# Optimization experiments

Measured on AMD Instinct MI355X. Metric: run time of the kernel, lower is better.

Reference implementation:

```python
import jax, jax.numpy as jnp
import numpy as np

NULL = -1.0
HORIZON = 10   # tile(1, 10, 1) in the original
N_REGIONS = 16


def setup_inputs() -> dict:
    key = jax.random.key(0)
    k1, k2, k3 = jax.random.split(key, 3)
    B, T, N, F = 16, 288, 4096, 2
    x = jax.random.uniform(k1, (B, T, N, F), dtype=jnp.float32) * 100.0
    miss = jax.random.uniform(k2, (B, T, N, F)) < 0.05
    x = jnp.where(miss, NULL, x)
    cluster_id = jax.random.randint(k3, (N,), 0, N_REGIONS)
    return {"data_seq": x, "cluster_id": cluster_id}


def reference(data_seq, cluster_id):
    # data_seq: [B, T, N, F] -> take feature 0 -> [B, T, N]
    x = data_seq[..., 0]
    # invalid_to_nan + nan_to_global_avg == replace -1 entries by global mean of valid entries
    valid = x != NULL
    xz = jnp.where(valid, x, 0.0)
    gmean = jnp.sum(xz) / jnp.maximum(jnp.sum(valid.astype(x.dtype)), 1.0)
    x = jnp.where(valid, x, gmean)
    # mean over time, tiled over prediction horizon: [B, HORIZON, N]
    pred_speed = jnp.tile(jnp.mean(x, axis=1, keepdims=True), (1, HORIZON, 1))
    # per-region mean over nodes (fused segment-mean instead of python loop): [B, HORIZON, R]
    counts = jax.ops.segment_sum(jnp.ones((cluster_id.shape[0],), x.dtype),
                                 cluster_id, num_segments=N_REGIONS)      # [R]
    sums = jax.ops.segment_sum(pred_speed.transpose(2, 0, 1),             # [N, B, H]
                               cluster_id, num_segments=N_REGIONS)        # [R, B, H]
    regional = (sums / jnp.maximum(counts, 1.0)[:, None, None]).transpose(1, 2, 0)
    return pred_speed, regional
```

## Files before the change

kernel.cpp:

```cpp
#include <hip/hip_runtime.h>
#include <hip/hip_bf16.h>

#define BB 16
#define TT 288
#define NN 4096
#define FF 2
#define RR 16
#define HH 10
#define TC 8
#define TSTEP (TT / TC)
#define NBLK1 (8 * TC * BB)
#define NULLV (-1.0f)

__global__ __launch_bounds__(256) void k_partial(
    const float4* __restrict__ x4,
    float2* __restrict__ psum2, int2* __restrict__ pcnt2,
    float* __restrict__ bsum, unsigned int* __restrict__ bcnt) {
  const int tid = threadIdx.x;
  const int n0  = blockIdx.x * 512 + tid * 2;
  const int tc  = blockIdx.y;
  const int b   = blockIdx.z;

  const float4* p = x4 + ((size_t)(b * TT + tc * TSTEP) * NN + n0) / 2;
  float s0 = 0.0f, s1 = 0.0f;
  unsigned int c0 = 0, c1 = 0;
#pragma unroll 12
  for (int t = 0; t < TSTEP; ++t) {
    float4 v = p[(size_t)t * (NN / 2)];
    bool v0 = (v.x != NULLV);
    bool v1 = (v.z != NULLV);
    s0 += v0 ? v.x : 0.0f;  c0 += v0 ? 1u : 0u;
    s1 += v1 ? v.z : 0.0f;  c1 += v1 ? 1u : 0u;
  }
  const size_t o2 = (((size_t)tc * BB + b) * NN + n0) / 2;
  psum2[o2] = make_float2(s0, s1);
  pcnt2[o2] = make_int2((int)c0, (int)c1);

  float rs = s0 + s1;
  unsigned int rc = c0 + c1;
  for (int off = 32; off > 0; off >>= 1) {
    rs += __shfl_down(rs, off);
    rc += __shfl_down(rc, off);
  }
  __shared__ float sh_s[4];
  __shared__ unsigned int sh_c[4];
  const int wid = tid >> 6;
  if ((tid & 63) == 0) { sh_s[wid] = rs; sh_c[wid] = rc; }
  __syncthreads();
  if (tid == 0) {
    const int blk = (blockIdx.z * TC + blockIdx.y) * 8 + blockIdx.x;
    bsum[blk] = sh_s[0] + sh_s[1] + sh_s[2] + sh_s[3];
    bcnt[blk] = sh_c[0] + sh_c[1] + sh_c[2] + sh_c[3];
  }
}

__global__ __launch_bounds__(256) void k_pred(
    const float4* __restrict__ psum4, const int4* __restrict__ pcnt4,
    const float4* __restrict__ bsum4, const uint4* __restrict__ bcnt4,
    const int4* __restrict__ cluster4,
    float4* __restrict__ out4, float* __restrict__ rsB) {
  const int tid = threadIdx.x;
  const int blk = blockIdx.x;
  const int b   = blk >> 2;
  const int n0  = (blk & 3) * 1024 + tid * 4;

  float4 bs = bsum4[tid];
  uint4  bc = bcnt4[tid];
  float rs = bs.x + bs.y + bs.z + bs.w;
  unsigned int rc = bc.x + bc.y + bc.z + bc.w;
  for (int off = 32; off > 0; off >>= 1) {
    rs += __shfl_down(rs, off);
    rc += __shfl_down(rc, off);
  }
  __shared__ float sh_s[4];
  __shared__ unsigned int sh_c[4];
  __shared__ float sh_gmean;
  const int wid = tid >> 6;
  if ((tid & 63) == 0) { sh_s[wid] = rs; sh_c[wid] = rc; }
  __syncthreads();
  if (tid == 0) {
    float gs = sh_s[0] + sh_s[1] + sh_s[2] + sh_s[3];
    float gc = (float)(sh_c[0] + sh_c[1] + sh_c[2] + sh_c[3]);
    sh_gmean = gs / fmaxf(gc, 1.0f);
  }
  __syncthreads();
  const float gmean = sh_gmean;

  float4 s = make_float4(0.f, 0.f, 0.f, 0.f);
  int4 c = make_int4(0, 0, 0, 0);
#pragma unroll
  for (int tc = 0; tc < TC; ++tc) {
    const size_t o4 = (((size_t)tc * BB + b) * NN + n0) / 4;
    float4 ps = psum4[o4];
    int4   pc = pcnt4[o4];
    s.x += ps.x; s.y += ps.y; s.z += ps.z; s.w += ps.w;
    c.x += pc.x; c.y += pc.y; c.z += pc.z; c.w += pc.w;
  }
  const float inv_t = 1.0f / (float)TT;
  float4 pred;
  pred.x = (s.x + (float)(TT - c.x) * gmean) * inv_t;
  pred.y = (s.y + (float)(TT - c.y) * gmean) * inv_t;
  pred.z = (s.z + (float)(TT - c.z) * gmean) * inv_t;
  pred.w = (s.w + (float)(TT - c.w) * gmean) * inv_t;

#pragma unroll
  for (int h = 0; h < HH; ++h)
    out4[((size_t)(b * HH + h) * NN + n0) / 4] = pred;

  __shared__ float rsh[RR];
  if (tid < RR) rsh[tid] = 0.0f;
  __syncthreads();
  int4 cl = cluster4[n0 / 4];
  atomicAdd(&rsh[cl.x], pred.x);
  atomicAdd(&rsh[cl.y], pred.y);
  atomicAdd(&rsh[cl.z], pred.z);
  atomicAdd(&rsh[cl.w], pred.w);
  __syncthreads();
  if (tid < RR) rsB[blk * RR + tid] = rsh[tid];
}

__global__ __launch_bounds__(256) void k_final(
    const int* __restrict__ cluster, const float* __restrict__ rsB,
    float* __restrict__ out2) {
  __shared__ unsigned int hist[RR];
  const int tid = threadIdx.x;
  if (tid < RR) hist[tid] = 0u;
  __syncthreads();
  for (int i = tid; i < NN; i += 256) atomicAdd(&hist[cluster[i]], 1u);
  __syncthreads();
  const int b = tid >> 4;
  const int r = tid & 15;
  float s = 0.0f;
#pragma unroll
  for (int q = 0; q < 4; ++q) s += rsB[((b << 2) + q) * RR + r];
  const float v = s / fmaxf((float)hist[r], 1.0f);
#pragma unroll
  for (int h = 0; h < HH; ++h)
    out2[(size_t)(b * HH + h) * RR + r] = v;
}

extern "C" void kernel_launch(void* const* d_in, const int* in_sizes, int n_in,
                              void* d_out, int out_size, void* d_ws, size_t ws_size,
                              hipStream_t stream) {
  const float* x       = (const float*)d_in[0];
  const int*   cluster = (const int*)d_in[1];
  float* out = (float*)d_out;

  float*        psum = (float*)d_ws;
  int*          pcnt = (int*)((char*)d_ws + (size_t)TC * BB * NN * 4);
  float*        bsum = (float*)((char*)d_ws + (size_t)2 * TC * BB * NN * 4);
  unsigned int* bcnt = (unsigned int*)((char*)bsum + 4096);
  float*        rsB  = (float*)((char*)bsum + 8192);

  dim3 g1(NN / 512, TC, BB);
  k_partial<<<g1, 256, 0, stream>>>((const float4*)x, (float2*)psum,
                                    (int2*)pcnt, bsum, bcnt);

  k_pred<<<64, 256, 0, stream>>>((const float4*)psum, (const int4*)pcnt,
                                 (const float4*)bsum, (const uint4*)bcnt,
                                 (const int4*)cluster, (float4*)out, rsB);

  k_final<<<1, 256, 0, stream>>>(cluster, rsB, out + (size_t)BB * HH * NN);
}
```

Before: 216.4 us.

## Fuse final regional reduction into pred kernel via last-block atomic counter

```diff
diff --git a/kernel.cpp b/kernel.cpp
--- a/kernel.cpp
+++ b/kernel.cpp
@@ -9,17 +9,23 @@
 #define HH 10
 #define TC 8
 #define TSTEP (TT / TC)
-#define NBLK1 (8 * TC * BB)
+#define NBLK2 64
 #define NULLV (-1.0f)
 
 __global__ __launch_bounds__(256) void k_partial(
     const float4* __restrict__ x4,
-    float2* __restrict__ psum2, int2* __restrict__ pcnt2,
-    float* __restrict__ bsum, unsigned int* __restrict__ bcnt) {
+    float4* __restrict__ ps4,
+    float* __restrict__ bsum, unsigned int* __restrict__ bcnt,
+    float* __restrict__ regsum, unsigned int* __restrict__ counter) {
   const int tid = threadIdx.x;
   const int n0  = blockIdx.x * 512 + tid * 2;
   const int tc  = blockIdx.y;
   const int b   = blockIdx.z;
+
+  if (blockIdx.x == 0 && tc == 0 && b == 0) {
+    regsum[tid] = 0.0f;
+    if (tid == 0) *counter = 0u;
+  }
 
   const float4* p = x4 + ((size_t)(b * TT + tc * TSTEP) * NN + n0) / 2;
   float s0 = 0.0f, s1 = 0.0f;
@@ -32,9 +38,8 @@
     s0 += v0 ? v.x : 0.0f;  c0 += v0 ? 1u : 0u;
     s1 += v1 ? v.z : 0.0f;  c1 += v1 ? 1u : 0u;
   }
-  const size_t o2 = (((size_t)tc * BB + b) * NN + n0) / 2;
-  psum2[o2] = make_float2(s0, s1);
-  pcnt2[o2] = make_int2((int)c0, (int)c1);
+  ps4[(((size_t)tc * BB + b) * NN + n0) / 2] =
+      make_float4(s0, (float)c0, s1, (float)c1);
 
   float rs = s0 + s1;
   unsigned int rc = c0 + c1;
@@ -55,10 +60,11 @@
 }
 
 __global__ __launch_bounds__(256) void k_pred(
-    const float4* __restrict__ psum4, const int4* __restrict__ pcnt4,
+    const float4* __restrict__ ps4,
     const float4* __restrict__ bsum4, const uint4* __restrict__ bcnt4,
-    const int4* __restrict__ cluster4,
-    float4* __restrict__ out4, float* __restrict__ rsB) {
+    const int4* __restrict__ cluster4, const int* __restrict__ cluster,
+    float4* __restrict__ out4, float* __restrict__ out2,
+    float* __restrict__ regsum, unsigned int* __restrict__ counter) {
   const int tid = threadIdx.x;
   const int blk = blockIdx.x;
   const int b   = blk >> 2;
@@ -87,21 +93,21 @@
   const float gmean = sh_gmean;
 
   float4 s = make_float4(0.f, 0.f, 0.f, 0.f);
-  int4 c = make_int4(0, 0, 0, 0);
+  float4 c = make_float4(0.f, 0.f, 0.f, 0.f);
 #pragma unroll
   for (int tc = 0; tc < TC; ++tc) {
-    const size_t o4 = (((size_t)tc * BB + b) * NN + n0) / 4;
-    float4 ps = psum4[o4];
-    int4   pc = pcnt4[o4];
-    s.x += ps.x; s.y += ps.y; s.z += ps.z; s.w += ps.w;
-    c.x += pc.x; c.y += pc.y; c.z += pc.z; c.w += pc.w;
+    const size_t o2 = (((size_t)tc * BB + b) * NN + n0) / 2;
+    float4 p0 = ps4[o2];
+    float4 p1 = ps4[o2 + 1];
+    s.x += p0.x; c.x += p0.y; s.y += p0.z; c.y += p0.w;
+    s.z += p1.x; c.z += p1.y; s.w += p1.z; c.w += p1.w;
   }
   const float inv_t = 1.0f / (float)TT;
   float4 pred;
-  pred.x = (s.x + (float)(TT - c.x) * gmean) * inv_t;
-  pred.y = (s.y + (float)(TT - c.y) * gmean) * inv_t;
-  pred.z = (s.z + (float)(TT - c.z) * gmean) * inv_t;
-  pred.w = (s.w + (float)(TT - c.w) * gmean) * inv_t;
+  pred.x = (s.x + ((float)TT - c.x) * gmean) * inv_t;
+  pred.y = (s.y + ((float)TT - c.y) * gmean) * inv_t;
+  pred.z = (s.z + ((float)TT - c.z) * gmean) * inv_t;
+  pred.w = (s.w + ((float)TT - c.w) * gmean) * inv_t;
 
 #pragma unroll
   for (int h = 0; h < HH; ++h)
@@ -116,27 +122,30 @@
   atomicAdd(&rsh[cl.z], pred.z);
   atomicAdd(&rsh[cl.w], pred.w);
   __syncthreads();
-  if (tid < RR) rsB[blk * RR + tid] = rsh[tid];
-}
+  if (tid < RR) atomicAdd(&regsum[b * RR + tid], rsh[tid]);
 
-__global__ __launch_bounds__(256) void k_final(
-    const int* __restrict__ cluster, const float* __restrict__ rsB,
-    float* __restrict__ out2) {
-  __shared__ unsigned int hist[RR];
-  const int tid = threadIdx.x;
-  if (tid < RR) hist[tid] = 0u;
+  __shared__ int sh_last;
+  __threadfence();
+  if (tid == 0) {
+    unsigned int old = atomicAdd(counter, 1u);
+    sh_last = (old == NBLK2 - 1) ? 1 : 0;
+  }
   __syncthreads();
-  for (int i = tid; i < NN; i += 256) atomicAdd(&hist[cluster[i]], 1u);
-  __syncthreads();
-  const int b = tid >> 4;
-  const int r = tid & 15;
-  float s = 0.0f;
+  if (sh_last) {
+    __threadfence();
+    __shared__ unsigned int hist[RR];
+    if (tid < RR) hist[tid] = 0u;
+    __syncthreads();
+    for (int i = tid; i < NN; i += 256) atomicAdd(&hist[cluster[i]], 1u);
+    __syncthreads();
+    const int ob = tid >> 4;
+    const int r  = tid & 15;
+    const float sreg = atomicAdd(&regsum[tid], 0.0f);
+    const float v = sreg / fmaxf((float)hist[r], 1.0f);
 #pragma unroll
-  for (int q = 0; q < 4; ++q) s += rsB[((b << 2) + q) * RR + r];
-  const float v = s / fmaxf((float)hist[r], 1.0f);
-#pragma unroll
-  for (int h = 0; h < HH; ++h)
-    out2[(size_t)(b * HH + h) * RR + r] = v;
+    for (int h = 0; h < HH; ++h)
+      out2[(size_t)(ob * HH + h) * RR + r] = v;
+  }
 }
 
 extern "C" void kernel_launch(void* const* d_in, const int* in_sizes, int n_in,
@@ -146,19 +155,19 @@
   const int*   cluster = (const int*)d_in[1];
   float* out = (float*)d_out;
 
-  float*        psum = (float*)d_ws;
-  int*          pcnt = (int*)((char*)d_ws + (size_t)TC * BB * NN * 4);
-  float*        bsum = (float*)((char*)d_ws + (size_t)2 * TC * BB * NN * 4);
-  unsigned int* bcnt = (unsigned int*)((char*)bsum + 4096);
-  float*        rsB  = (float*)((char*)bsum + 8192);
+  float*        ps      = (float*)d_ws;
+  float*        bsum    = (float*)((char*)d_ws + (size_t)TC * BB * NN * 8);
+  unsigned int* bcnt    = (unsigned int*)((char*)bsum + 4096);
+  float*        regsum  = (float*)((char*)bsum + 8192);
+  unsigned int* counter = (unsigned int*)((char*)bsum + 12288);
 
   dim3 g1(NN / 512, TC, BB);
-  k_partial<<<g1, 256, 0, stream>>>((const float4*)x, (float2*)psum,
-                                    (int2*)pcnt, bsum, bcnt);
+  k_partial<<<g1, 256, 0, stream>>>((const float4*)x, (float4*)ps,
+                                    bsum, bcnt, regsum, counter);
 
-  k_pred<<<64, 256, 0, stream>>>((const float4*)psum, (const int4*)pcnt,
-                                 (const float4*)bsum, (const uint4*)bcnt,
-                                 (const int4*)cluster, (float4*)out, rsB);
-
-  k_final<<<1, 256, 0, stream>>>(cluster, rsB, out + (size_t)BB * HH * NN);
+  k_pred<<<NBLK2, 256, 0, stream>>>((const float4*)ps,
+                                    (const float4*)bsum, (const uint4*)bcnt,
+                                    (const int4*)cluster, cluster,
+                                    (float4*)out, out + (size_t)BB * HH * NN,
+                                    regsum, counter);
 }
```

Result: slower. 220.8 us (+2.0%).
